# Performance work log

Measured on AMD Instinct MI355X. Metric: run time of the kernel, lower is better.

The kernel has to match this reference:

```python
import jax, jax.numpy as jnp
import numpy as np

# model config (see init_kwargs)
L, H, NH, KVH, DH, I, P, F, T = 8, 1024, 16, 2, 64, 4096, 4, 64, 10
QLEN = 9                      # 1 dit token + P cond tokens + P latent tokens
GROUPS = NH // KVH            # GQA repeat factor
PREFIX = P + 1                # prefix_plus
SCALE = DH ** -0.25           # folded into rope cos/sin (applied to q AND k)


def setup_inputs() -> dict:
    key = jax.random.key(0)
    ks = jax.random.split(key, 16)
    g = lambda i, shape, s=0.02: jax.random.normal(ks[i], shape, jnp.float32) * s
    # sway-sampled timestep schedule -> dt table (matches torch precompute)
    ts = np.linspace(1.0, 0.0, T + 1, dtype=np.float32)
    ts = (ts + 1.0 * (np.cos(np.pi / 2 * ts) - 1.0 + ts))[1:]
    dt_all = jnp.asarray((ts[:-1] - ts[1:]).reshape(1, 1, T - 1))
    # rope tables with attention scale folded in
    pos = np.arange(QLEN, dtype=np.float32)
    inv_freq = 1.0 / (10000.0 ** (np.arange(0, DH, 2, dtype=np.float32) / DH))
    freqs = np.concatenate([np.outer(pos, inv_freq)] * 2, axis=-1)  # [QLEN, DH]
    cos_q = jnp.asarray(np.cos(freqs)[None, None] * SCALE)  # [1,1,QLEN,DH]
    sin_q = jnp.asarray(np.sin(freqs)[None, None] * SCALE)
    return dict(
        random=g(0, (1, P, F), 1.0),
        dit_hidden=g(1, (1, 1, H), 1.0),
        feat_cond=g(2, (2, P, H), 1.0),
        cfg_value=jnp.full((1,), 2.5, jnp.float32),
        cfg_value_minus=jnp.full((1,), -1.5, jnp.float32),
        t_all=g(3, (1, T - 1, H), 1.0),   # precomputed time_mlp output table
        dt_all=dt_all, cos_q=cos_q, sin_q=sin_q,
        W_in=g(4, (F, H)), b_in=jnp.zeros((H,), jnp.float32),
        ln1_w=jnp.ones((L, H), jnp.float32),
        Wq=g(5, (L, H, NH * DH)), Wk=g(6, (L, H, KVH * DH)),
        Wv=g(7, (L, H, KVH * DH)), Wo=g(8, (L, NH * DH, H)),
        ln2_w=jnp.ones((L, H), jnp.float32),
        Wg=g(9, (L, H, I)), Wu=g(10, (L, H, I)), Wd=g(11, (L, I, H)),
        norm_w=jnp.ones((H,), jnp.float32),
        W_out=g(12, (H, F)), b_out=jnp.zeros((F,), jnp.float32),
        step=jnp.zeros((1,), jnp.int32),
    )


def _rms(x, w, eps=1e-6):
    return x * jax.lax.rsqrt(jnp.mean(x * x, axis=-1, keepdims=True) + eps) * w


def _rot_half(x):
    x1, x2 = jnp.split(x, 2, axis=-1)
    return jnp.concatenate([-x2, x1], axis=-1)


def reference(random, dit_hidden, feat_cond, cfg_value, cfg_value_minus,
              t_all, dt_all, cos_q, sin_q, W_in, b_in, ln1_w, Wq, Wk, Wv, Wo,
              ln2_w, Wg, Wu, Wd, norm_w, W_out, b_out, step):
    t = t_all[:, step]                                   # [1,1,H]
    dt = dt_all[..., step]                               # [1,1,1]
    dh = jnp.concatenate([dit_hidden + t, t], axis=0)    # CFG doubling -> [2,1,H]
    x = random @ W_in + b_in                             # [1,P,H]
    h = jnp.concatenate([dh, feat_cond, jnp.concatenate([x, x], axis=0)], axis=1)  # [2,QLEN,H]

    def layer(h, p):
        ln1, wq, wk, wv, wo, ln2, wg, wu, wd = p
        hn = _rms(h, ln1)
        q = (hn @ wq).reshape(2, QLEN, NH, DH).transpose(0, 2, 1, 3)
        k = (hn @ wk).reshape(2, QLEN, KVH, DH).transpose(0, 2, 1, 3)
        v = (hn @ wv).reshape(2, QLEN, KVH, DH).transpose(0, 2, 1, 3)
        # rope with head_dim**-0.25 scale folded into cos/sin (applied to q and k)
        q = q * cos_q + _rot_half(q) * sin_q
        k = k * cos_q + _rot_half(k) * sin_q
        k = jnp.repeat(k, GROUPS, axis=1)                # repeat_k (GQA)
        v = jnp.repeat(v, GROUPS, axis=1)                # repeat_v
        attn = jax.nn.softmax(jnp.einsum('bhqd,bhkd->bhqk', q, k), axis=-1)
        out = jnp.einsum('bhqk,bhkd->bhqd', attn, v)
        out = out.transpose(0, 2, 1, 3).reshape(2, QLEN, NH * DH)
        h = h + out @ wo
        hn2 = _rms(h, ln2)
        h = h + (jax.nn.silu(hn2 @ wg) * (hn2 @ wu)) @ wd
        return h, None

    h, _ = jax.lax.scan(layer, h, (ln1_w, Wq, Wk, Wv, Wo, ln2_w, Wg, Wu, Wd))
    h = _rms(h[:, PREFIX:], norm_w)                      # drop prefix -> [2,P,H]
    out = h @ W_out + b_out                              # [2,P,F]
    pos, neg = out[0:1], out[1:2]
    pf = pos.reshape(1, 1, -1)                           # [1,1,P*F]
    nf = neg.reshape(1, -1, 1)                           # [1,P*F,1]
    st = (pf @ nf) / (jnp.swapaxes(nf, 1, 2) @ nf + 1e-7)  # rescaled CFG, [1,1,1]
    dphi = cfg_value_minus * neg * st + cfg_value * pos
    next_random = random - dt * dphi
    return step + 1, next_random
```

## Files before the change

### kernel.cpp

```cpp
#include <hip/hip_runtime.h>

#define TOKENS 18
#define QLEN 9
#define HDIM 1024
#define IDIM 4096
#define NLAYER 8

#define HA_OFF    0u
#define HB_OFF    18432u
#define SQA_OFF   36864u
#define SQB_OFF   36936u
#define QKVR_OFF  37008u
#define QKVP_OFF  60048u
#define OPP_OFF   797328u
#define GUP_OFF   1387152u
#define M_OFF     3746448u
#define WDP_OFF   3820176u
#define OUTP_OFF  4999824u
#define TOTAL_F   5016208u

__device__ __forceinline__ void loadf2(float2* buf, const float* wp, int base, int stride) {
#pragma unroll
  for (int j = 0; j < 8; j++)
    buf[j] = *reinterpret_cast<const float2*>(wp + (size_t)(base + j) * stride);
}
__device__ __forceinline__ void fmaf2(float2* acc, const float2* buf,
                                      const float (*sb)[TOKENS], int base) {
#pragma unroll
  for (int j = 0; j < 8; j++) {
#pragma unroll
    for (int t = 0; t < TOKENS; t++) {
      float bv = sb[base + j][t];
      acc[t].x += bv * buf[j].x; acc[t].y += bv * buf[j].y;
    }
  }
}
__device__ __forceinline__ void loadf1(float* buf, const float* wp, int base, int stride) {
#pragma unroll
  for (int j = 0; j < 8; j++) buf[j] = wp[(size_t)(base + j) * stride];
}
__device__ __forceinline__ void fmaf1(float* acc, const float* buf,
                                      const float (*sb)[TOKENS], int base) {
#pragma unroll
  for (int j = 0; j < 8; j++) {
#pragma unroll
    for (int t = 0; t < TOKENS; t++) acc[t] += sb[base + j][t] * buf[j];
  }
}

__global__ __launch_bounds__(256) void k_embed(
    const float* __restrict__ rnd, const float* __restrict__ dit,
    const float* __restrict__ feat, const float* __restrict__ t_all,
    const float* __restrict__ W_in, const float* __restrict__ b_in,
    const int* __restrict__ step, float* __restrict__ ws) {
  int t = blockIdx.x >> 2, q4 = blockIdx.x & 3, c0 = q4 * 256;
  int b = t / QLEN, q = t - b * QLEN;
  int tid = threadIdx.x, c = c0 + tid;
  int st = step[0];
  __shared__ float rl[64];
  __shared__ float pr[4];
  float v;
  if (q == 0) {
    v = t_all[(size_t)st * HDIM + c] + (b == 0 ? dit[c] : 0.f);
  } else if (q <= 4) {
    v = feat[(size_t)(b * 4 + q - 1) * HDIM + c];
  } else {
    int p = q - 5;
    if (tid < 64) rl[tid] = rnd[p * 64 + tid];
    __syncthreads();
    float a = b_in[c];
#pragma unroll 8
    for (int f = 0; f < 64; f++) a += rl[f] * W_in[(size_t)f * HDIM + c];
    v = a;
  }
  ws[HA_OFF + (size_t)t * HDIM + c] = v;
  float sq = v * v;
#pragma unroll
  for (int off = 32; off >= 1; off >>= 1) sq += __shfl_down(sq, off);
  if ((tid & 63) == 0) pr[tid >> 6] = sq;
  __syncthreads();
  if (tid == 0) ws[SQA_OFF + (size_t)t * 4 + q4] = pr[0] + pr[1] + pr[2] + pr[3];
}

__global__ __launch_bounds__(256) void k_qkv(
    const float* __restrict__ Wq, const float* __restrict__ Wk,
    const float* __restrict__ Wv, const float* __restrict__ ln1,
    float* __restrict__ ws, int layer) {
  int ks = blockIdx.y, r0 = ks * 32, bx = blockIdx.x, tid = threadIdx.x;
  __shared__ float s_b[32][TOKENS];
  __shared__ float s_rstd[TOKENS];
  if (tid < TOKENS) {
    float s = ws[SQA_OFF + tid * 4] + ws[SQA_OFF + tid * 4 + 1]
            + ws[SQA_OFF + tid * 4 + 2] + ws[SQA_OFF + tid * 4 + 3];
    s_rstd[tid] = rsqrtf(s * (1.f / HDIM) + 1e-6f);
  }
  const float* lw = ln1 + (size_t)layer * HDIM;
  for (int i = tid; i < 576; i += 256) {
    int t = i >> 5, r = i & 31;
    s_b[r][t] = ws[HA_OFF + (size_t)t * HDIM + r0 + r] * lw[r0 + r];
  }
  __syncthreads();
  float* qp = ws + QKVP_OFF + (size_t)ks * (TOKENS * 1280);
  if (bx < 2) {
    int col = bx * 512 + tid * 2;
    const float* wp = Wq + ((size_t)layer << 20) + (size_t)r0 * HDIM + col;
    float2 A[8], B[8];
    float2 acc[TOKENS];
#pragma unroll
    for (int t = 0; t < TOKENS; t++) acc[t] = make_float2(0.f, 0.f);
    loadf2(A, wp, 0, HDIM); loadf2(B, wp, 8, HDIM);
    fmaf2(acc, A, s_b, 0);  loadf2(A, wp, 16, HDIM);
    fmaf2(acc, B, s_b, 8);  loadf2(B, wp, 24, HDIM);
    fmaf2(acc, A, s_b, 16); fmaf2(acc, B, s_b, 24);
#pragma unroll
    for (int t = 0; t < TOKENS; t++) {
      float rs = s_rstd[t];
      *reinterpret_cast<float2*>(qp + (size_t)t * 1280 + col) = make_float2(acc[t].x * rs, acc[t].y * rs);
    }
  } else {
    int c = tid;
    const float* wp = (c < 128)
      ? (Wk + (size_t)layer * 131072 + (size_t)r0 * 128 + c)
      : (Wv + (size_t)layer * 131072 + (size_t)r0 * 128 + (c - 128));
    float A[8], B[8];
    float acc[TOKENS];
#pragma unroll
    for (int t = 0; t < TOKENS; t++) acc[t] = 0.f;
    loadf1(A, wp, 0, 128); loadf1(B, wp, 8, 128);
    fmaf1(acc, A, s_b, 0);  loadf1(A, wp, 16, 128);
    fmaf1(acc, B, s_b, 8);  loadf1(B, wp, 24, 128);
    fmaf1(acc, A, s_b, 16); fmaf1(acc, B, s_b, 24);
#pragma unroll
    for (int t = 0; t < TOKENS; t++) qp[(size_t)t * 1280 + 1024 + c] = acc[t] * s_rstd[t];
  }
}

__global__ __launch_bounds__(256) void k_redq(float* __restrict__ ws) {
  int el = blockIdx.x * 256 + threadIdx.x;
  float s = 0.f;
#pragma unroll 8
  for (int p = 0; p < 32; p++) s += ws[QKVP_OFF + (size_t)p * (TOKENS * 1280) + el];
  ws[QKVR_OFF + el] = s;
}

__global__ __launch_bounds__(256) void k_wo(
    const float* __restrict__ Wo, const float* __restrict__ cosq,
    const float* __restrict__ sinq, float* __restrict__ ws, int layer) {
  const float* qkv = ws + QKVR_OFF;
  int bx = blockIdx.x, by = blockIdx.y, tid = threadIdx.x;
  int r0 = by * 32, head = r0 >> 6, kvh = head >> 3, d0 = r0 & 63;
  __shared__ float lq[2][QLEN][68];
  __shared__ float lk[2][QLEN][68];
  __shared__ float lv[2][QLEN][33];
  __shared__ float sP[2][QLEN][12];
  __shared__ float sA[32][TOKENS];
  for (int i = tid; i < 2 * QLEN * 64; i += 256) {
    int d = i & 63, qi = (i >> 6) % QLEN, b = i / (QLEN * 64);
    const float* qr = qkv + (size_t)(b * QLEN + qi) * 1280;
    float c = cosq[qi * 64 + d], s = sinq[qi * 64 + d];
    float qv = qr[head * 64 + d];
    float qo = (d < 32) ? -qr[head * 64 + d + 32] : qr[head * 64 + d - 32];
    lq[b][qi][d] = qv * c + qo * s;
    float kv = qr[1024 + kvh * 64 + d];
    float ko = (d < 32) ? -qr[1024 + kvh * 64 + d + 32] : qr[1024 + kvh * 64 + d - 32];
    lk[b][qi][d] = kv * c + ko * s;
  }
  for (int i = tid; i < 2 * QLEN * 32; i += 256) {
    int d = i & 31, ki = (i >> 5) % QLEN, b = i / (QLEN * 32);
    lv[b][ki][d] = qkv[(size_t)(b * QLEN + ki) * 1280 + 1152 + kvh * 64 + d0 + d];
  }
  __syncthreads();
  for (int i = tid; i < 2 * QLEN * QLEN; i += 256) {
    int ki = i % QLEN, qi = (i / QLEN) % QLEN, b = i / (QLEN * QLEN);
    float s = 0.f;
#pragma unroll
    for (int d = 0; d < 64; d++) s += lq[b][qi][d] * lk[b][ki][d];
    sP[b][qi][ki] = s;
  }
  __syncthreads();
  if (tid < TOKENS) {
    int b = tid / QLEN, qi = tid % QLEN;
    float m = -1e30f;
#pragma unroll
    for (int k = 0; k < QLEN; k++) m = fmaxf(m, sP[b][qi][k]);
    float e[QLEN], sum = 0.f;
#pragma unroll
    for (int k = 0; k < QLEN; k++) { e[k] = expf(sP[b][qi][k] - m); sum += e[k]; }
    float inv = 1.f / sum;
#pragma unroll
    for (int k = 0; k < QLEN; k++) sP[b][qi][k] = e[k] * inv;
  }
  __syncthreads();
  for (int i = tid; i < 32 * TOKENS; i += 256) {
    int dd = i / TOKENS, t = i - dd * TOKENS;
    int b = t / QLEN, qi = t % QLEN;
    float a = 0.f;
#pragma unroll
    for (int k = 0; k < QLEN; k++) a += sP[b][qi][k] * lv[b][k][dd];
    sA[dd][t] = a;
  }
  __syncthreads();
  int col = bx * 512 + tid * 2;
  const float* wp = Wo + ((size_t)layer << 20) + (size_t)r0 * HDIM + col;
  float2 A[8], B[8];
  float2 acc[TOKENS];
#pragma unroll
  for (int t = 0; t < TOKENS; t++) acc[t] = make_float2(0.f, 0.f);
  loadf2(A, wp, 0, HDIM); loadf2(B, wp, 8, HDIM);
  fmaf2(acc, A, sA, 0);   loadf2(A, wp, 16, HDIM);
  fmaf2(acc, B, sA, 8);   loadf2(B, wp, 24, HDIM);
  fmaf2(acc, A, sA, 16);  fmaf2(acc, B, sA, 24);
  float* op = ws + OPP_OFF + (size_t)by * (TOKENS * HDIM);
#pragma unroll
  for (int t = 0; t < TOKENS; t++)
    *reinterpret_cast<float2*>(op + (size_t)t * HDIM + col) = acc[t];
}

__global__ __launch_bounds__(256) void k_redo(float* __restrict__ ws) {
  int t = blockIdx.x >> 2, q4 = blockIdx.x & 3;
  int tid = threadIdx.x, c = q4 * 256 + tid;
  __shared__ float pr[4];
  float v = ws[HA_OFF + (size_t)t * HDIM + c];
  const float* pp = ws + OPP_OFF + (size_t)t * HDIM + c;
#pragma unroll 8
  for (int p = 0; p < 32; p++) v += pp[(size_t)p * (TOKENS * HDIM)];
  ws[HB_OFF + (size_t)t * HDIM + c] = v;
  float sq = v * v;
#pragma unroll
  for (int off = 32; off >= 1; off >>= 1) sq += __shfl_down(sq, off);
  if ((tid & 63) == 0) pr[tid >> 6] = sq;
  __syncthreads();
  if (tid == 0) ws[SQB_OFF + (size_t)t * 4 + q4] = pr[0] + pr[1] + pr[2] + pr[3];
}

__global__ __launch_bounds__(256) void k_gu(
    const float* __restrict__ Wg, const float* __restrict__ Wu,
    const float* __restrict__ ln2, float* __restrict__ ws, int layer) {
  int cs = blockIdx.x, ks = blockIdx.y, r0 = ks * 64, tid = threadIdx.x;
  __shared__ float s_b[TOKENS][64];
  __shared__ float s_rstd[TOKENS];
  if (tid < TOKENS) {
    float s = ws[SQB_OFF + tid * 4] + ws[SQB_OFF + tid * 4 + 1]
            + ws[SQB_OFF + tid * 4 + 2] + ws[SQB_OFF + tid * 4 + 3];
    s_rstd[tid] = rsqrtf(s * (1.f / HDIM) + 1e-6f);
  }
  const float* lw = ln2 + (size_t)layer * HDIM;
  for (int i = tid; i < TOKENS * 64; i += 256) {
    int t = i >> 6, r = i & 63;
    s_b[t][r] = ws[HB_OFF + (size_t)t * HDIM + r0 + r] * lw[r0 + r];
  }
  __syncthreads();
  const float* W = (cs < 16 ? Wg : Wu) + ((size_t)layer << 22);
  int base = (cs & 15) * 256;
  const float* wp = W + (size_t)r0 * IDIM + base + tid;
  float wbuf[64];
#pragma unroll
  for (int j = 0; j < 64; j++) wbuf[j] = wp[(size_t)j * IDIM];
  float acc[TOKENS];
#pragma unroll
  for (int t = 0; t < TOKENS; t++) acc[t] = 0.f;
#pragma unroll
  for (int j = 0; j < 64; j++) {
#pragma unroll
    for (int t = 0; t < TOKENS; t++) acc[t] += s_b[t][j] * wbuf[j];
  }
  int outcol = (cs < 16 ? base : 4096 + base) + tid;
  float* gp = ws + GUP_OFF + (size_t)ks * (TOKENS * 8192) + outcol;
#pragma unroll
  for (int t = 0; t < TOKENS; t++) gp[(size_t)t * 8192] = acc[t] * s_rstd[t];
}

__global__ __launch_bounds__(256) void k_m(float* __restrict__ ws) {
  int el = blockIdx.x * 256 + threadIdx.x;
  int t = el >> 12, j = el & 4095;
  const float* gp = ws + GUP_OFF + (size_t)t * 8192 + j;
  float g = 0.f, u = 0.f;
#pragma unroll 8
  for (int p = 0; p < 16; p++) {
    g += gp[(size_t)p * (TOKENS * 8192)];
    u += gp[(size_t)p * (TOKENS * 8192) + 4096];
  }
  ws[M_OFF + (size_t)t * 4096 + j] = (g / (1.f + expf(-g))) * u;
}

__global__ __launch_bounds__(256) void k_wd(
    const float* __restrict__ Wd, float* __restrict__ ws, int layer) {
  int ks2 = blockIdx.x >> 3, cs = blockIdx.x & 7;
  int r0 = ks2 * 128, c0 = cs * 128;
  int tid = threadIdx.x, colt = tid & 127, hf = tid >> 7;
  __shared__ float s_b[TOKENS][128];
  for (int i = tid; i < TOKENS * 128; i += 256) {
    int t = i >> 7, r = i & 127;
    s_b[t][r] = ws[M_OFF + (size_t)t * 4096 + r0 + r];
  }
  __syncthreads();
  int col = c0 + colt;
  const float* wp = Wd + ((size_t)layer << 22) + (size_t)(r0 + hf * 64) * HDIM + col;
  float wbuf[64];
#pragma unroll
  for (int j = 0; j < 64; j++) wbuf[j] = wp[(size_t)j * HDIM];
  float acc[TOKENS];
#pragma unroll
  for (int t = 0; t < TOKENS; t++) acc[t] = 0.f;
#pragma unroll
  for (int j = 0; j < 64; j++) {
#pragma unroll
    for (int t = 0; t < TOKENS; t++) acc[t] += s_b[t][hf * 64 + j] * wbuf[j];
  }
  int slab = ks2 * 2 + hf;
  float* wdp = ws + WDP_OFF + (size_t)slab * (TOKENS * HDIM) + col;
#pragma unroll
  for (int t = 0; t < TOKENS; t++) wdp[(size_t)t * HDIM] = acc[t];
}

__global__ __launch_bounds__(256) void k_hup(float* __restrict__ ws) {
  int t = blockIdx.x >> 2, q4 = blockIdx.x & 3;
  int tid = threadIdx.x, c = q4 * 256 + tid;
  __shared__ float pr[4];
  float v = ws[HB_OFF + (size_t)t * HDIM + c];
  const float* pp = ws + WDP_OFF + (size_t)t * HDIM + c;
#pragma unroll 8
  for (int p = 0; p < 64; p++) v += pp[(size_t)p * (TOKENS * HDIM)];
  ws[HA_OFF + (size_t)t * HDIM + c] = v;
  float sq = v * v;
#pragma unroll
  for (int off = 32; off >= 1; off >>= 1) sq += __shfl_down(sq, off);
  if ((tid & 63) == 0) pr[tid >> 6] = sq;
  __syncthreads();
  if (tid == 0) ws[SQA_OFF + (size_t)t * 4 + q4] = pr[0] + pr[1] + pr[2] + pr[3];
}

__global__ __launch_bounds__(256) void k_out(
    const float* __restrict__ Wout, const float* __restrict__ normw,
    float* __restrict__ ws) {
  const float* h = ws + HA_OFF;
  float* outp = ws + OUTP_OFF;
  __shared__ float s_rstd[8];
  __shared__ float s_b[128][8];
  int tid = threadIdx.x;
  if (tid < 8) {
    int tix = (tid >> 2) * QLEN + 5 + (tid & 3);
    float s = ws[SQA_OFF + tix * 4] + ws[SQA_OFF + tix * 4 + 1]
            + ws[SQA_OFF + tix * 4 + 2] + ws[SQA_OFF + tix * 4 + 3];
    s_rstd[tid] = rsqrtf(s * (1.f / HDIM) + 1e-6f);
  }
  __syncthreads();
  int r0 = blockIdx.x * 128;
  for (int i = tid; i < 128 * 8; i += 256) {
    int r = i >> 3, s = i & 7;
    int tix = (s >> 2) * QLEN + 5 + (s & 3);
    s_b[r][s] = h[(size_t)tix * HDIM + r0 + r] * normw[r0 + r] * s_rstd[s];
  }
  __syncthreads();
  int colc = tid & 63, rsub = tid >> 6;
  const float* wp = Wout + (size_t)(r0 + rsub * 32) * 64 + colc;
  float acc[8];
#pragma unroll
  for (int s = 0; s < 8; s++) acc[s] = 0.f;
#pragma unroll 8
  for (int r = 0; r < 32; r++) {
    float w = wp[(size_t)r * 64];
#pragma unroll
    for (int s = 0; s < 8; s++) acc[s] += s_b[rsub * 32 + r][s] * w;
  }
  float* slot = outp + (size_t)(blockIdx.x * 4 + rsub) * 512;
#pragma unroll
  for (int s = 0; s < 8; s++) slot[s * 64 + colc] = acc[s];
}

__global__ __launch_bounds__(256) void k_final(
    const float* __restrict__ rnd, const float* __restrict__ cfg,
    const float* __restrict__ cfgm, const float* __restrict__ dt_all,
    const float* __restrict__ bout, const int* __restrict__ step,
    const float* __restrict__ ws, float* __restrict__ out) {
  const float* outp = ws + OUTP_OFF;
  int tid = threadIdx.x;
  int f = tid & 63;
  float p = bout[f], n = bout[f];
#pragma unroll 8
  for (int pp = 0; pp < 32; pp++) {
    p += outp[(size_t)pp * 512 + tid];
    n += outp[(size_t)pp * 512 + 256 + tid];
  }
  float pn = p * n, nn = n * n;
#pragma unroll
  for (int off = 32; off >= 1; off >>= 1) {
    pn += __shfl_down(pn, off);
    nn += __shfl_down(nn, off);
  }
  __shared__ float red[8];
  __shared__ float s_st;
  int wave = tid >> 6, lane = tid & 63;
  if (lane == 0) { red[wave] = pn; red[4 + wave] = nn; }
  __syncthreads();
  if (tid == 0) {
    float PN = red[0] + red[1] + red[2] + red[3];
    float NN = red[4] + red[5] + red[6] + red[7];
    s_st = PN / (NN + 1e-7f);
  }
  __syncthreads();
  int st = step[0];
  float dphi = cfgm[0] * n * s_st + cfg[0] * p;
  float next = rnd[tid] - dt_all[st] * dphi;
  if (tid == 0) out[0] = (float)(st + 1);
  out[1 + tid] = next;
}

extern "C" void kernel_launch(void* const* d_in, const int* in_sizes, int n_in,
                              void* d_out, int out_size, void* d_ws, size_t ws_size,
                              hipStream_t stream) {
  const float* rnd   = (const float*)d_in[0];
  const float* dit   = (const float*)d_in[1];
  const float* feat  = (const float*)d_in[2];
  const float* cfg   = (const float*)d_in[3];
  const float* cfgm  = (const float*)d_in[4];
  const float* t_all = (const float*)d_in[5];
  const float* dt_al = (const float*)d_in[6];
  const float* cosq  = (const float*)d_in[7];
  const float* sinq  = (const float*)d_in[8];
  const float* W_in  = (const float*)d_in[9];
  const float* b_in  = (const float*)d_in[10];
  const float* ln1   = (const float*)d_in[11];
  const float* Wq    = (const float*)d_in[12];
  const float* Wk    = (const float*)d_in[13];
  const float* Wv    = (const float*)d_in[14];
  const float* Wo    = (const float*)d_in[15];
  const float* ln2   = (const float*)d_in[16];
  const float* Wg    = (const float*)d_in[17];
  const float* Wu    = (const float*)d_in[18];
  const float* Wd    = (const float*)d_in[19];
  const float* normw = (const float*)d_in[20];
  const float* Wout  = (const float*)d_in[21];
  const float* bout  = (const float*)d_in[22];
  const int*   step  = (const int*)d_in[23];
  float* ws = (float*)d_ws;

  k_embed<<<72, 256, 0, stream>>>(rnd, dit, feat, t_all, W_in, b_in, step, ws);
  for (int l = 0; l < NLAYER; l++) {
    k_qkv<<<dim3(3, 32), 256, 0, stream>>>(Wq, Wk, Wv, ln1, ws, l);
    k_redq<<<90, 256, 0, stream>>>(ws);
    k_wo<<<dim3(2, 32), 256, 0, stream>>>(Wo, cosq, sinq, ws, l);
    k_redo<<<72, 256, 0, stream>>>(ws);
    k_gu<<<dim3(32, 16), 256, 0, stream>>>(Wg, Wu, ln2, ws, l);
    k_m<<<288, 256, 0, stream>>>(ws);
    k_wd<<<256, 256, 0, stream>>>(Wd, ws, l);
    k_hup<<<72, 256, 0, stream>>>(ws);
  }
  k_out<<<8, 256, 0, stream>>>(Wout, normw, ws);
  k_final<<<1, 256, 0, stream>>>(rnd, cfg, cfgm, dt_al, bout, step, ws, (float*)d_out);
}
```

Before: 550.3 us.

## Fuse split-K reductions into consumer kernels with in-kernel atomic flag sync

Removes the separate reduction kernels (redq, redo, and per-layer hup). Their work moves into the first 72 blocks of the next kernel, which publish completion through agent-scope atomic counters. The other blocks prefetch their weights into registers before spinning on the counter, so weight loads overlap the reduction. QKV and Wo now use larger 64-row K-slices, giving fewer partials and the wo kernel sums the QKV partials itself. This cuts launches, but it relies on all producer blocks being co-resident or scheduled first to avoid deadlock, and the wider register buffers raise register pressure.

```diff
diff --git a/kernel.cpp b/kernel.cpp
--- a/kernel.cpp
+++ b/kernel.cpp
@@ -10,42 +10,22 @@
 #define HB_OFF    18432u
 #define SQA_OFF   36864u
 #define SQB_OFF   36936u
-#define QKVR_OFF  37008u
-#define QKVP_OFF  60048u
-#define OPP_OFF   797328u
-#define GUP_OFF   1387152u
-#define M_OFF     3746448u
-#define WDP_OFF   3820176u
-#define OUTP_OFF  4999824u
-#define TOTAL_F   5016208u
-
-__device__ __forceinline__ void loadf2(float2* buf, const float* wp, int base, int stride) {
-#pragma unroll
-  for (int j = 0; j < 8; j++)
-    buf[j] = *reinterpret_cast<const float2*>(wp + (size_t)(base + j) * stride);
-}
-__device__ __forceinline__ void fmaf2(float2* acc, const float2* buf,
-                                      const float (*sb)[TOKENS], int base) {
-#pragma unroll
-  for (int j = 0; j < 8; j++) {
-#pragma unroll
-    for (int t = 0; t < TOKENS; t++) {
-      float bv = sb[base + j][t];
-      acc[t].x += bv * buf[j].x; acc[t].y += bv * buf[j].y;
-    }
-  }
-}
-__device__ __forceinline__ void loadf1(float* buf, const float* wp, int base, int stride) {
-#pragma unroll
-  for (int j = 0; j < 8; j++) buf[j] = wp[(size_t)(base + j) * stride];
-}
-__device__ __forceinline__ void fmaf1(float* acc, const float* buf,
-                                      const float (*sb)[TOKENS], int base) {
-#pragma unroll
-  for (int j = 0; j < 8; j++) {
-#pragma unroll
-    for (int t = 0; t < TOKENS; t++) acc[t] += sb[base + j][t] * buf[j];
-  }
+#define CNT_OFF   37008u
+#define QKVP_OFF  37072u
+#define OPP_OFF   405712u
+#define GUP_OFF   700624u
+#define M_OFF     3059920u
+#define WDP_OFF   3133648u
+#define OUTP_OFF  4313296u
+#define TOTAL_F   4329680u
+
+__device__ __forceinline__ void flag_release(unsigned* c) {
+  __threadfence();
+  __hip_atomic_fetch_add(c, 1u, __ATOMIC_RELEASE, __HIP_MEMORY_SCOPE_AGENT);
+}
+__device__ __forceinline__ void flag_spin(unsigned* c, unsigned tgt) {
+  while (__hip_atomic_load(c, __ATOMIC_ACQUIRE, __HIP_MEMORY_SCOPE_AGENT) < tgt)
+    __builtin_amdgcn_s_sleep(2);
 }
 
 __global__ __launch_bounds__(256) void k_embed(
@@ -79,95 +59,122 @@
   for (int off = 32; off >= 1; off >>= 1) sq += __shfl_down(sq, off);
   if ((tid & 63) == 0) pr[tid >> 6] = sq;
   __syncthreads();
-  if (tid == 0) ws[SQA_OFF + (size_t)t * 4 + q4] = pr[0] + pr[1] + pr[2] + pr[3];
+  if (tid == 0) {
+    ws[SQA_OFF + (size_t)t * 4 + q4] = pr[0] + pr[1] + pr[2] + pr[3];
+    flag_release((unsigned*)(ws + CNT_OFF) + 0);
+  }
 }
 
 __global__ __launch_bounds__(256) void k_qkv(
     const float* __restrict__ Wq, const float* __restrict__ Wk,
     const float* __restrict__ Wv, const float* __restrict__ ln1,
     float* __restrict__ ws, int layer) {
-  int ks = blockIdx.y, r0 = ks * 32, bx = blockIdx.x, tid = threadIdx.x;
-  __shared__ float s_b[32][TOKENS];
+  int bx = blockIdx.x, ks = blockIdx.y, r0 = ks * 64, tid = threadIdx.x;
+  int id = ks * 5 + bx;
+  unsigned* cnt = (unsigned*)(ws + CNT_OFF) + layer;
+  __shared__ float s_b[64][TOKENS];
   __shared__ float s_rstd[TOKENS];
+  __shared__ float pr[4];
+  if (layer > 0 && id < 72) {
+    int t = id >> 2, q4 = id & 3, c = q4 * 256 + tid;
+    float v = ws[HB_OFF + (size_t)t * HDIM + c];
+    const float* pp = ws + WDP_OFF + (size_t)t * HDIM + c;
+#pragma unroll 8
+    for (int p = 0; p < 64; p++) v += pp[(size_t)p * (TOKENS * HDIM)];
+    ws[HA_OFF + (size_t)t * HDIM + c] = v;
+    float sq = v * v;
+#pragma unroll
+    for (int off = 32; off >= 1; off >>= 1) sq += __shfl_down(sq, off);
+    if ((tid & 63) == 0) pr[tid >> 6] = sq;
+    __syncthreads();
+    if (tid == 0) {
+      ws[SQA_OFF + (size_t)t * 4 + q4] = pr[0] + pr[1] + pr[2] + pr[3];
+      flag_release(cnt);
+    }
+  }
+  float W[64];
+  const float* wp;
+  int stride;
+  int col = 0;
+  if (bx < 4) {
+    col = bx * 256 + tid;
+    wp = Wq + ((size_t)layer << 20) + (size_t)r0 * HDIM + col;
+    stride = HDIM;
+  } else {
+    wp = (tid < 128)
+       ? (Wk + (size_t)layer * 131072 + (size_t)r0 * 128 + tid)
+       : (Wv + (size_t)layer * 131072 + (size_t)r0 * 128 + (tid - 128));
+    stride = 128;
+  }
+#pragma unroll
+  for (int j = 0; j < 64; j++) W[j] = wp[(size_t)j * stride];
+  if (tid == 0) flag_spin(cnt, 72u);
+  __syncthreads();
   if (tid < TOKENS) {
     float s = ws[SQA_OFF + tid * 4] + ws[SQA_OFF + tid * 4 + 1]
             + ws[SQA_OFF + tid * 4 + 2] + ws[SQA_OFF + tid * 4 + 3];
     s_rstd[tid] = rsqrtf(s * (1.f / HDIM) + 1e-6f);
   }
   const float* lw = ln1 + (size_t)layer * HDIM;
-  for (int i = tid; i < 576; i += 256) {
-    int t = i >> 5, r = i & 31;
+  for (int i = tid; i < 64 * TOKENS; i += 256) {
+    int t = i % TOKENS, r = i / TOKENS;
     s_b[r][t] = ws[HA_OFF + (size_t)t * HDIM + r0 + r] * lw[r0 + r];
   }
   __syncthreads();
+  float acc[TOKENS];
+#pragma unroll
+  for (int t = 0; t < TOKENS; t++) acc[t] = 0.f;
+#pragma unroll
+  for (int j = 0; j < 64; j++) {
+#pragma unroll
+    for (int t = 0; t < TOKENS; t++) acc[t] += s_b[j][t] * W[j];
+  }
   float* qp = ws + QKVP_OFF + (size_t)ks * (TOKENS * 1280);
-  if (bx < 2) {
-    int col = bx * 512 + tid * 2;
-    const float* wp = Wq + ((size_t)layer << 20) + (size_t)r0 * HDIM + col;
-    float2 A[8], B[8];
-    float2 acc[TOKENS];
-#pragma unroll
-    for (int t = 0; t < TOKENS; t++) acc[t] = make_float2(0.f, 0.f);
-    loadf2(A, wp, 0, HDIM); loadf2(B, wp, 8, HDIM);
-    fmaf2(acc, A, s_b, 0);  loadf2(A, wp, 16, HDIM);
-    fmaf2(acc, B, s_b, 8);  loadf2(B, wp, 24, HDIM);
-    fmaf2(acc, A, s_b, 16); fmaf2(acc, B, s_b, 24);
-#pragma unroll
-    for (int t = 0; t < TOKENS; t++) {
-      float rs = s_rstd[t];
-      *reinterpret_cast<float2*>(qp + (size_t)t * 1280 + col) = make_float2(acc[t].x * rs, acc[t].y * rs);
-    }
+  if (bx < 4) {
+#pragma unroll
+    for (int t = 0; t < TOKENS; t++) qp[(size_t)t * 1280 + col] = acc[t] * s_rstd[t];
   } else {
-    int c = tid;
-    const float* wp = (c < 128)
-      ? (Wk + (size_t)layer * 131072 + (size_t)r0 * 128 + c)
-      : (Wv + (size_t)layer * 131072 + (size_t)r0 * 128 + (c - 128));
-    float A[8], B[8];
-    float acc[TOKENS];
-#pragma unroll
-    for (int t = 0; t < TOKENS; t++) acc[t] = 0.f;
-    loadf1(A, wp, 0, 128); loadf1(B, wp, 8, 128);
-    fmaf1(acc, A, s_b, 0);  loadf1(A, wp, 16, 128);
-    fmaf1(acc, B, s_b, 8);  loadf1(B, wp, 24, 128);
-    fmaf1(acc, A, s_b, 16); fmaf1(acc, B, s_b, 24);
-#pragma unroll
-    for (int t = 0; t < TOKENS; t++) qp[(size_t)t * 1280 + 1024 + c] = acc[t] * s_rstd[t];
-  }
-}
-
-__global__ __launch_bounds__(256) void k_redq(float* __restrict__ ws) {
-  int el = blockIdx.x * 256 + threadIdx.x;
-  float s = 0.f;
-#pragma unroll 8
-  for (int p = 0; p < 32; p++) s += ws[QKVP_OFF + (size_t)p * (TOKENS * 1280) + el];
-  ws[QKVR_OFF + el] = s;
+#pragma unroll
+    for (int t = 0; t < TOKENS; t++) qp[(size_t)t * 1280 + 1024 + tid] = acc[t] * s_rstd[t];
+  }
 }
 
 __global__ __launch_bounds__(256) void k_wo(
     const float* __restrict__ Wo, const float* __restrict__ cosq,
     const float* __restrict__ sinq, float* __restrict__ ws, int layer) {
-  const float* qkv = ws + QKVR_OFF;
   int bx = blockIdx.x, by = blockIdx.y, tid = threadIdx.x;
-  int r0 = by * 32, head = r0 >> 6, kvh = head >> 3, d0 = r0 & 63;
+  int head = by, kvh = head >> 3;
   __shared__ float lq[2][QLEN][68];
   __shared__ float lk[2][QLEN][68];
-  __shared__ float lv[2][QLEN][33];
+  __shared__ float lv[2][QLEN][68];
   __shared__ float sP[2][QLEN][12];
-  __shared__ float sA[32][TOKENS];
+  __shared__ float sA[64][TOKENS];
   for (int i = tid; i < 2 * QLEN * 64; i += 256) {
     int d = i & 63, qi = (i >> 6) % QLEN, b = i / (QLEN * 64);
-    const float* qr = qkv + (size_t)(b * QLEN + qi) * 1280;
-    float c = cosq[qi * 64 + d], s = sinq[qi * 64 + d];
-    float qv = qr[head * 64 + d];
-    float qo = (d < 32) ? -qr[head * 64 + d + 32] : qr[head * 64 + d - 32];
-    lq[b][qi][d] = qv * c + qo * s;
-    float kv = qr[1024 + kvh * 64 + d];
-    float ko = (d < 32) ? -qr[1024 + kvh * 64 + d + 32] : qr[1024 + kvh * 64 + d - 32];
-    lk[b][qi][d] = kv * c + ko * s;
-  }
+    const float* base = ws + QKVP_OFF + (size_t)(b * QLEN + qi) * 1280;
+    float qs = 0.f, ks2 = 0.f, vs = 0.f;
+#pragma unroll 8
+    for (int p = 0; p < 16; p++) {
+      const float* sp = base + (size_t)p * (TOKENS * 1280);
+      qs  += sp[head * 64 + d];
+      ks2 += sp[1024 + kvh * 64 + d];
+      vs  += sp[1152 + kvh * 64 + d];
+    }
+    lq[b][qi][d] = qs;
+    lk[b][qi][d] = ks2;
+    lv[b][qi][d] = vs;
+  }
+  __syncthreads();
   for (int i = tid; i < 2 * QLEN * 32; i += 256) {
-    int d = i & 31, ki = (i >> 5) % QLEN, b = i / (QLEN * 32);
-    lv[b][ki][d] = qkv[(size_t)(b * QLEN + ki) * 1280 + 1152 + kvh * 64 + d0 + d];
+    int d = i & 31, qi = (i >> 5) % QLEN, b = i / (QLEN * 32);
+    float c1 = cosq[qi * 64 + d],      s1 = sinq[qi * 64 + d];
+    float c2 = cosq[qi * 64 + 32 + d], s2 = sinq[qi * 64 + 32 + d];
+    float qa = lq[b][qi][d], qb = lq[b][qi][32 + d];
+    lq[b][qi][d]      = qa * c1 - qb * s1;
+    lq[b][qi][32 + d] = qb * c2 + qa * s2;
+    float ka = lk[b][qi][d], kb = lk[b][qi][32 + d];
+    lk[b][qi][d]      = ka * c1 - kb * s1;
+    lk[b][qi][32 + d] = kb * c2 + ka * s2;
   }
   __syncthreads();
   for (int i = tid; i < 2 * QLEN * QLEN; i += 256) {
@@ -191,8 +198,8 @@
     for (int k = 0; k < QLEN; k++) sP[b][qi][k] = e[k] * inv;
   }
   __syncthreads();
-  for (int i = tid; i < 32 * TOKENS; i += 256) {
-    int dd = i / TOKENS, t = i - dd * TOKENS;
+  for (int i = tid; i < 64 * TOKENS; i += 256) {
+    int dd = i / TOKENS, t = i % TOKENS;
     int b = t / QLEN, qi = t % QLEN;
     float a = 0.f;
 #pragma unroll
@@ -200,45 +207,58 @@
     sA[dd][t] = a;
   }
   __syncthreads();
-  int col = bx * 512 + tid * 2;
-  const float* wp = Wo + ((size_t)layer << 20) + (size_t)r0 * HDIM + col;
-  float2 A[8], B[8];
-  float2 acc[TOKENS];
-#pragma unroll
-  for (int t = 0; t < TOKENS; t++) acc[t] = make_float2(0.f, 0.f);
-  loadf2(A, wp, 0, HDIM); loadf2(B, wp, 8, HDIM);
-  fmaf2(acc, A, sA, 0);   loadf2(A, wp, 16, HDIM);
-  fmaf2(acc, B, sA, 8);   loadf2(B, wp, 24, HDIM);
-  fmaf2(acc, A, sA, 16);  fmaf2(acc, B, sA, 24);
+  int col = bx * 256 + tid;
+  const float* wp = Wo + ((size_t)layer << 20) + (size_t)(head * 64) * HDIM + col;
+  float W[64];
+#pragma unroll
+  for (int j = 0; j < 64; j++) W[j] = wp[(size_t)j * HDIM];
+  float acc[TOKENS];
+#pragma unroll
+  for (int t = 0; t < TOKENS; t++) acc[t] = 0.f;
+#pragma unroll
+  for (int j = 0; j < 64; j++) {
+#pragma unroll
+    for (int t = 0; t < TOKENS; t++) acc[t] += sA[j][t] * W[j];
+  }
   float* op = ws + OPP_OFF + (size_t)by * (TOKENS * HDIM);
 #pragma unroll
-  for (int t = 0; t < TOKENS; t++)
-    *reinterpret_cast<float2*>(op + (size_t)t * HDIM + col) = acc[t];
-}
-
-__global__ __launch_bounds__(256) void k_redo(float* __restrict__ ws) {
-  int t = blockIdx.x >> 2, q4 = blockIdx.x & 3;
-  int tid = threadIdx.x, c = q4 * 256 + tid;
-  __shared__ float pr[4];
-  float v = ws[HA_OFF + (size_t)t * HDIM + c];
-  const float* pp = ws + OPP_OFF + (size_t)t * HDIM + c;
-#pragma unroll 8
-  for (int p = 0; p < 32; p++) v += pp[(size_t)p * (TOKENS * HDIM)];
-  ws[HB_OFF + (size_t)t * HDIM + c] = v;
-  float sq = v * v;
-#pragma unroll
-  for (int off = 32; off >= 1; off >>= 1) sq += __shfl_down(sq, off);
-  if ((tid & 63) == 0) pr[tid >> 6] = sq;
-  __syncthreads();
-  if (tid == 0) ws[SQB_OFF + (size_t)t * 4 + q4] = pr[0] + pr[1] + pr[2] + pr[3];
-}
-
-__global__ __launch_bounds__(256) void k_gu(
+  for (int t = 0; t < TOKENS; t++) op[(size_t)t * HDIM + col] = acc[t];
+}
+
+__global__ __launch_bounds__(256, 2) void k_gu(
     const float* __restrict__ Wg, const float* __restrict__ Wu,
     const float* __restrict__ ln2, float* __restrict__ ws, int layer) {
-  int cs = blockIdx.x, ks = blockIdx.y, r0 = ks * 64, tid = threadIdx.x;
+  int bid = blockIdx.x, tid = threadIdx.x;
+  int cs = bid >> 4, ks = bid & 15, r0 = ks * 64;
+  unsigned* cnt = (unsigned*)(ws + CNT_OFF) + 8 + layer;
   __shared__ float s_b[TOKENS][64];
   __shared__ float s_rstd[TOKENS];
+  __shared__ float pr[4];
+  if (bid < 72) {
+    int t = bid >> 2, q4 = bid & 3, c = q4 * 256 + tid;
+    float v = ws[HA_OFF + (size_t)t * HDIM + c];
+    const float* pp = ws + OPP_OFF + (size_t)t * HDIM + c;
+#pragma unroll 8
+    for (int p = 0; p < 16; p++) v += pp[(size_t)p * (TOKENS * HDIM)];
+    ws[HB_OFF + (size_t)t * HDIM + c] = v;
+    float sq = v * v;
+#pragma unroll
+    for (int off = 32; off >= 1; off >>= 1) sq += __shfl_down(sq, off);
+    if ((tid & 63) == 0) pr[tid >> 6] = sq;
+    __syncthreads();
+    if (tid == 0) {
+      ws[SQB_OFF + (size_t)t * 4 + q4] = pr[0] + pr[1] + pr[2] + pr[3];
+      flag_release(cnt);
+    }
+  }
+  int base = (cs & 15) * 256;
+  const float* W = (cs < 16 ? Wg : Wu) + ((size_t)layer << 22);
+  const float* wp = W + (size_t)r0 * IDIM + base + tid;
+  float wbuf[64];
+#pragma unroll
+  for (int j = 0; j < 64; j++) wbuf[j] = wp[(size_t)j * IDIM];
+  if (tid == 0) flag_spin(cnt, 72u);
+  __syncthreads();
   if (tid < TOKENS) {
     float s = ws[SQB_OFF + tid * 4] + ws[SQB_OFF + tid * 4 + 1]
             + ws[SQB_OFF + tid * 4 + 2] + ws[SQB_OFF + tid * 4 + 3];
@@ -250,12 +270,6 @@
     s_b[t][r] = ws[HB_OFF + (size_t)t * HDIM + r0 + r] * lw[r0 + r];
   }
   __syncthreads();
-  const float* W = (cs < 16 ? Wg : Wu) + ((size_t)layer << 22);
-  int base = (cs & 15) * 256;
-  const float* wp = W + (size_t)r0 * IDIM + base + tid;
-  float wbuf[64];
-#pragma unroll
-  for (int j = 0; j < 64; j++) wbuf[j] = wp[(size_t)j * IDIM];
   float acc[TOKENS];
 #pragma unroll
   for (int t = 0; t < TOKENS; t++) acc[t] = 0.f;
@@ -435,17 +449,17 @@
   const int*   step  = (const int*)d_in[23];
   float* ws = (float*)d_ws;
 
+  hipMemsetAsync((void*)(ws + CNT_OFF), 0, 64 * sizeof(unsigned), stream);
+
   k_embed<<<72, 256, 0, stream>>>(rnd, dit, feat, t_all, W_in, b_in, step, ws);
   for (int l = 0; l < NLAYER; l++) {
-    k_qkv<<<dim3(3, 32), 256, 0, stream>>>(Wq, Wk, Wv, ln1, ws, l);
-    k_redq<<<90, 256, 0, stream>>>(ws);
-    k_wo<<<dim3(2, 32), 256, 0, stream>>>(Wo, cosq, sinq, ws, l);
-    k_redo<<<72, 256, 0, stream>>>(ws);
-    k_gu<<<dim3(32, 16), 256, 0, stream>>>(Wg, Wu, ln2, ws, l);
+    k_qkv<<<dim3(5, 16), 256, 0, stream>>>(Wq, Wk, Wv, ln1, ws, l);
+    k_wo<<<dim3(4, 16), 256, 0, stream>>>(Wo, cosq, sinq, ws, l);
+    k_gu<<<512, 256, 0, stream>>>(Wg, Wu, ln2, ws, l);
     k_m<<<288, 256, 0, stream>>>(ws);
     k_wd<<<256, 256, 0, stream>>>(Wd, ws, l);
-    k_hup<<<72, 256, 0, stream>>>(ws);
-  }
+  }
+  k_hup<<<72, 256, 0, stream>>>(ws);
   k_out<<<8, 256, 0, stream>>>(Wout, normw, ws);
   k_final<<<1, 256, 0, stream>>>(rnd, cfg, cfgm, dt_al, bout, step, ws, (float*)d_out);
 }
```

After: 821.3 us. 1.49x slower.

## Fold split-K reductions into GEMV kernels and fuse SiLU-gate into down-proj

Applied to the files above, without the earlier changes.

The QKV, gate/up and down projection kernels now have each block stage the full normalized activation vector in LDS and reduce over K inside the block, using wave shuffles and a small LDS reduction. This removes the separate split-K partial-sum kernels (k_redq, k_m) and shrinks the partial buffers. The SiLU*up product is now computed inside k_wd from the gate/up outputs. The cost is that every block reloads and renormalizes the whole 1024x18 activation tile into about 72KB of LDS, which limits occupancy and duplicates that prologue work. Weight reads also move to 16-column-wide strided patterns with less coalescing per row.

```diff
diff --git a/kernel.cpp b/kernel.cpp
--- a/kernel.cpp
+++ b/kernel.cpp
@@ -11,13 +11,11 @@
 #define SQA_OFF   36864u
 #define SQB_OFF   36936u
 #define QKVR_OFF  37008u
-#define QKVP_OFF  60048u
-#define OPP_OFF   797328u
-#define GUP_OFF   1387152u
-#define M_OFF     3746448u
-#define WDP_OFF   3820176u
-#define OUTP_OFF  4999824u
-#define TOTAL_F   5016208u
+#define OPP_OFF   60048u
+#define GU_OFF    649872u
+#define WDP_OFF   797328u
+#define OUTP_OFF  871056u
+#define TOTAL_F   887440u
 
 __device__ __forceinline__ void loadf2(float2* buf, const float* wp, int base, int stride) {
 #pragma unroll
@@ -33,18 +31,6 @@
       float bv = sb[base + j][t];
       acc[t].x += bv * buf[j].x; acc[t].y += bv * buf[j].y;
     }
-  }
-}
-__device__ __forceinline__ void loadf1(float* buf, const float* wp, int base, int stride) {
-#pragma unroll
-  for (int j = 0; j < 8; j++) buf[j] = wp[(size_t)(base + j) * stride];
-}
-__device__ __forceinline__ void fmaf1(float* acc, const float* buf,
-                                      const float (*sb)[TOKENS], int base) {
-#pragma unroll
-  for (int j = 0; j < 8; j++) {
-#pragma unroll
-    for (int t = 0; t < TOKENS; t++) acc[t] += sb[base + j][t] * buf[j];
   }
 }
 
@@ -86,61 +72,62 @@
     const float* __restrict__ Wq, const float* __restrict__ Wk,
     const float* __restrict__ Wv, const float* __restrict__ ln1,
     float* __restrict__ ws, int layer) {
-  int ks = blockIdx.y, r0 = ks * 32, bx = blockIdx.x, tid = threadIdx.x;
-  __shared__ float s_b[32][TOKENS];
+  int blk = blockIdx.x, tid = threadIdx.x;
+  int seg = tid >> 4, col = tid & 15;
+  __shared__ float hn[1024 * TOKENS];
+  __shared__ float red[4 * 16 * TOKENS];
   __shared__ float s_rstd[TOKENS];
   if (tid < TOKENS) {
     float s = ws[SQA_OFF + tid * 4] + ws[SQA_OFF + tid * 4 + 1]
             + ws[SQA_OFF + tid * 4 + 2] + ws[SQA_OFF + tid * 4 + 3];
     s_rstd[tid] = rsqrtf(s * (1.f / HDIM) + 1e-6f);
   }
+  __syncthreads();
   const float* lw = ln1 + (size_t)layer * HDIM;
-  for (int i = tid; i < 576; i += 256) {
-    int t = i >> 5, r = i & 31;
-    s_b[r][t] = ws[HA_OFF + (size_t)t * HDIM + r0 + r] * lw[r0 + r];
-  }
-  __syncthreads();
-  float* qp = ws + QKVP_OFF + (size_t)ks * (TOKENS * 1280);
-  if (bx < 2) {
-    int col = bx * 512 + tid * 2;
-    const float* wp = Wq + ((size_t)layer << 20) + (size_t)r0 * HDIM + col;
-    float2 A[8], B[8];
-    float2 acc[TOKENS];
-#pragma unroll
-    for (int t = 0; t < TOKENS; t++) acc[t] = make_float2(0.f, 0.f);
-    loadf2(A, wp, 0, HDIM); loadf2(B, wp, 8, HDIM);
-    fmaf2(acc, A, s_b, 0);  loadf2(A, wp, 16, HDIM);
-    fmaf2(acc, B, s_b, 8);  loadf2(B, wp, 24, HDIM);
-    fmaf2(acc, A, s_b, 16); fmaf2(acc, B, s_b, 24);
-#pragma unroll
-    for (int t = 0; t < TOKENS; t++) {
-      float rs = s_rstd[t];
-      *reinterpret_cast<float2*>(qp + (size_t)t * 1280 + col) = make_float2(acc[t].x * rs, acc[t].y * rs);
+#pragma unroll 2
+  for (int t = 0; t < TOKENS; t++) {
+    float rs = s_rstd[t];
+    for (int row = tid; row < 1024; row += 256)
+      hn[row * TOKENS + t] = ws[HA_OFF + (size_t)t * HDIM + row] * lw[row] * rs;
+  }
+  __syncthreads();
+  int c0 = blk * 16;
+  const float* wp; int stride;
+  if (c0 < 1024)      { wp = Wq + ((size_t)layer << 20) + (size_t)(seg * 64) * 1024 + c0 + col; stride = 1024; }
+  else if (c0 < 1152) { wp = Wk + (size_t)layer * 131072 + (size_t)(seg * 64) * 128 + (c0 - 1024) + col; stride = 128; }
+  else                { wp = Wv + (size_t)layer * 131072 + (size_t)(seg * 64) * 128 + (c0 - 1152) + col; stride = 128; }
+  float acc[TOKENS];
+#pragma unroll
+  for (int t = 0; t < TOKENS; t++) acc[t] = 0.f;
+#pragma unroll
+  for (int jc = 0; jc < 8; jc++) {
+    float wb[8];
+#pragma unroll
+    for (int j = 0; j < 8; j++) wb[j] = wp[(size_t)(jc * 8 + j) * stride];
+#pragma unroll
+    for (int j = 0; j < 8; j++) {
+      const float* hr = &hn[(seg * 64 + jc * 8 + j) * TOKENS];
+#pragma unroll
+      for (int t = 0; t < TOKENS; t++) acc[t] += hr[t] * wb[j];
     }
-  } else {
-    int c = tid;
-    const float* wp = (c < 128)
-      ? (Wk + (size_t)layer * 131072 + (size_t)r0 * 128 + c)
-      : (Wv + (size_t)layer * 131072 + (size_t)r0 * 128 + (c - 128));
-    float A[8], B[8];
-    float acc[TOKENS];
-#pragma unroll
-    for (int t = 0; t < TOKENS; t++) acc[t] = 0.f;
-    loadf1(A, wp, 0, 128); loadf1(B, wp, 8, 128);
-    fmaf1(acc, A, s_b, 0);  loadf1(A, wp, 16, 128);
-    fmaf1(acc, B, s_b, 8);  loadf1(B, wp, 24, 128);
-    fmaf1(acc, A, s_b, 16); fmaf1(acc, B, s_b, 24);
-#pragma unroll
-    for (int t = 0; t < TOKENS; t++) qp[(size_t)t * 1280 + 1024 + c] = acc[t] * s_rstd[t];
-  }
-}
-
-__global__ __launch_bounds__(256) void k_redq(float* __restrict__ ws) {
-  int el = blockIdx.x * 256 + threadIdx.x;
-  float s = 0.f;
-#pragma unroll 8
-  for (int p = 0; p < 32; p++) s += ws[QKVP_OFF + (size_t)p * (TOKENS * 1280) + el];
-  ws[QKVR_OFF + el] = s;
+  }
+#pragma unroll
+  for (int t = 0; t < TOKENS; t++) {
+    acc[t] += __shfl_down(acc[t], 32);
+    acc[t] += __shfl_down(acc[t], 16);
+  }
+  int lane = tid & 63, wv = tid >> 6;
+  if (lane < 16) {
+#pragma unroll
+    for (int t = 0; t < TOKENS; t++) red[(wv * 16 + lane) * TOKENS + t] = acc[t];
+  }
+  __syncthreads();
+  for (int i = tid; i < 16 * TOKENS; i += 256) {
+    int c = i & 15, t = i >> 4;
+    float s = red[(0 * 16 + c) * TOKENS + t] + red[(1 * 16 + c) * TOKENS + t]
+            + red[(2 * 16 + c) * TOKENS + t] + red[(3 * 16 + c) * TOKENS + t];
+    ws[QKVR_OFF + (size_t)t * 1280 + c0 + c] = s;
+  }
 }
 
 __global__ __launch_bounds__(256) void k_wo(
@@ -233,84 +220,116 @@
   if (tid == 0) ws[SQB_OFF + (size_t)t * 4 + q4] = pr[0] + pr[1] + pr[2] + pr[3];
 }
 
-__global__ __launch_bounds__(256) void k_gu(
+__global__ __launch_bounds__(256) void k_gum(
     const float* __restrict__ Wg, const float* __restrict__ Wu,
     const float* __restrict__ ln2, float* __restrict__ ws, int layer) {
-  int cs = blockIdx.x, ks = blockIdx.y, r0 = ks * 64, tid = threadIdx.x;
-  __shared__ float s_b[TOKENS][64];
+  int b = blockIdx.x, tid = threadIdx.x;
+  int mat = b >> 8, j0 = (b & 255) * 16;
+  int seg = tid >> 4, col = tid & 15;
+  __shared__ float hn[1024 * TOKENS];
+  __shared__ float red[4 * 16 * TOKENS];
   __shared__ float s_rstd[TOKENS];
   if (tid < TOKENS) {
     float s = ws[SQB_OFF + tid * 4] + ws[SQB_OFF + tid * 4 + 1]
             + ws[SQB_OFF + tid * 4 + 2] + ws[SQB_OFF + tid * 4 + 3];
     s_rstd[tid] = rsqrtf(s * (1.f / HDIM) + 1e-6f);
   }
+  __syncthreads();
   const float* lw = ln2 + (size_t)layer * HDIM;
-  for (int i = tid; i < TOKENS * 64; i += 256) {
-    int t = i >> 6, r = i & 63;
-    s_b[t][r] = ws[HB_OFF + (size_t)t * HDIM + r0 + r] * lw[r0 + r];
-  }
-  __syncthreads();
-  const float* W = (cs < 16 ? Wg : Wu) + ((size_t)layer << 22);
-  int base = (cs & 15) * 256;
-  const float* wp = W + (size_t)r0 * IDIM + base + tid;
-  float wbuf[64];
-#pragma unroll
-  for (int j = 0; j < 64; j++) wbuf[j] = wp[(size_t)j * IDIM];
+#pragma unroll 2
+  for (int t = 0; t < TOKENS; t++) {
+    float rs = s_rstd[t];
+    for (int row = tid; row < 1024; row += 256)
+      hn[row * TOKENS + t] = ws[HB_OFF + (size_t)t * HDIM + row] * lw[row] * rs;
+  }
+  __syncthreads();
+  const float* wp = (mat ? Wu : Wg) + ((size_t)layer << 22)
+                  + (size_t)(seg * 64) * IDIM + j0 + col;
   float acc[TOKENS];
 #pragma unroll
   for (int t = 0; t < TOKENS; t++) acc[t] = 0.f;
 #pragma unroll
-  for (int j = 0; j < 64; j++) {
-#pragma unroll
-    for (int t = 0; t < TOKENS; t++) acc[t] += s_b[t][j] * wbuf[j];
-  }
-  int outcol = (cs < 16 ? base : 4096 + base) + tid;
-  float* gp = ws + GUP_OFF + (size_t)ks * (TOKENS * 8192) + outcol;
-#pragma unroll
-  for (int t = 0; t < TOKENS; t++) gp[(size_t)t * 8192] = acc[t] * s_rstd[t];
-}
-
-__global__ __launch_bounds__(256) void k_m(float* __restrict__ ws) {
-  int el = blockIdx.x * 256 + threadIdx.x;
-  int t = el >> 12, j = el & 4095;
-  const float* gp = ws + GUP_OFF + (size_t)t * 8192 + j;
-  float g = 0.f, u = 0.f;
-#pragma unroll 8
-  for (int p = 0; p < 16; p++) {
-    g += gp[(size_t)p * (TOKENS * 8192)];
-    u += gp[(size_t)p * (TOKENS * 8192) + 4096];
-  }
-  ws[M_OFF + (size_t)t * 4096 + j] = (g / (1.f + expf(-g))) * u;
+  for (int jc = 0; jc < 8; jc++) {
+    float wb[8];
+#pragma unroll
+    for (int j = 0; j < 8; j++) wb[j] = wp[(size_t)(jc * 8 + j) * IDIM];
+#pragma unroll
+    for (int j = 0; j < 8; j++) {
+      const float* hr = &hn[(seg * 64 + jc * 8 + j) * TOKENS];
+#pragma unroll
+      for (int t = 0; t < TOKENS; t++) acc[t] += hr[t] * wb[j];
+    }
+  }
+#pragma unroll
+  for (int t = 0; t < TOKENS; t++) {
+    acc[t] += __shfl_down(acc[t], 32);
+    acc[t] += __shfl_down(acc[t], 16);
+  }
+  int lane = tid & 63, wv = tid >> 6;
+  if (lane < 16) {
+#pragma unroll
+    for (int t = 0; t < TOKENS; t++) red[(wv * 16 + lane) * TOKENS + t] = acc[t];
+  }
+  __syncthreads();
+  for (int i = tid; i < 16 * TOKENS; i += 256) {
+    int c = i & 15, t = i >> 4;
+    float s = red[(0 * 16 + c) * TOKENS + t] + red[(1 * 16 + c) * TOKENS + t]
+            + red[(2 * 16 + c) * TOKENS + t] + red[(3 * 16 + c) * TOKENS + t];
+    ws[GU_OFF + (size_t)t * 8192 + mat * 4096 + j0 + c] = s;
+  }
 }
 
 __global__ __launch_bounds__(256) void k_wd(
     const float* __restrict__ Wd, float* __restrict__ ws, int layer) {
-  int ks2 = blockIdx.x >> 3, cs = blockIdx.x & 7;
-  int r0 = ks2 * 128, c0 = cs * 128;
-  int tid = threadIdx.x, colt = tid & 127, hf = tid >> 7;
-  __shared__ float s_b[TOKENS][128];
-  for (int i = tid; i < TOKENS * 128; i += 256) {
-    int t = i >> 7, r = i & 127;
-    s_b[t][r] = ws[M_OFF + (size_t)t * 4096 + r0 + r];
-  }
-  __syncthreads();
-  int col = c0 + colt;
-  const float* wp = Wd + ((size_t)layer << 22) + (size_t)(r0 + hf * 64) * HDIM + col;
-  float wbuf[64];
-#pragma unroll
-  for (int j = 0; j < 64; j++) wbuf[j] = wp[(size_t)j * HDIM];
+  int b = blockIdx.x, tid = threadIdx.x;
+  int kc = b >> 6, cc = b & 63;
+  int k0 = kc * 1024, c0 = cc * 16;
+  int seg = tid >> 4, col = tid & 15;
+  __shared__ float mt[1024 * TOKENS];
+  __shared__ float red[4 * 16 * TOKENS];
+#pragma unroll 2
+  for (int t = 0; t < TOKENS; t++) {
+    for (int row = tid; row < 1024; row += 256) {
+      float g = ws[GU_OFF + (size_t)t * 8192 + k0 + row];
+      float u = ws[GU_OFF + (size_t)t * 8192 + 4096 + k0 + row];
+      mt[row * TOKENS + t] = (g / (1.f + expf(-g))) * u;
+    }
+  }
+  __syncthreads();
+  const float* wp = Wd + ((size_t)layer << 22)
+                  + (size_t)(k0 + seg * 64) * HDIM + c0 + col;
   float acc[TOKENS];
 #pragma unroll
   for (int t = 0; t < TOKENS; t++) acc[t] = 0.f;
 #pragma unroll
-  for (int j = 0; j < 64; j++) {
-#pragma unroll
-    for (int t = 0; t < TOKENS; t++) acc[t] += s_b[t][hf * 64 + j] * wbuf[j];
-  }
-  int slab = ks2 * 2 + hf;
-  float* wdp = ws + WDP_OFF + (size_t)slab * (TOKENS * HDIM) + col;
-#pragma unroll
-  for (int t = 0; t < TOKENS; t++) wdp[(size_t)t * HDIM] = acc[t];
+  for (int jc = 0; jc < 8; jc++) {
+    float wb[8];
+#pragma unroll
+    for (int j = 0; j < 8; j++) wb[j] = wp[(size_t)(jc * 8 + j) * HDIM];
+#pragma unroll
+    for (int j = 0; j < 8; j++) {
+      const float* hr = &mt[(seg * 64 + jc * 8 + j) * TOKENS];
+#pragma unroll
+      for (int t = 0; t < TOKENS; t++) acc[t] += hr[t] * wb[j];
+    }
+  }
+#pragma unroll
+  for (int t = 0; t < TOKENS; t++) {
+    acc[t] += __shfl_down(acc[t], 32);
+    acc[t] += __shfl_down(acc[t], 16);
+  }
+  int lane = tid & 63, wv = tid >> 6;
+  if (lane < 16) {
+#pragma unroll
+    for (int t = 0; t < TOKENS; t++) red[(wv * 16 + lane) * TOKENS + t] = acc[t];
+  }
+  __syncthreads();
+  for (int i = tid; i < 16 * TOKENS; i += 256) {
+    int c = i & 15, t = i >> 4;
+    float s = red[(0 * 16 + c) * TOKENS + t] + red[(1 * 16 + c) * TOKENS + t]
+            + red[(2 * 16 + c) * TOKENS + t] + red[(3 * 16 + c) * TOKENS + t];
+    ws[WDP_OFF + (size_t)kc * (TOKENS * HDIM) + (size_t)t * HDIM + c0 + c] = s;
+  }
 }
 
 __global__ __launch_bounds__(256) void k_hup(float* __restrict__ ws) {
@@ -319,8 +338,8 @@
   __shared__ float pr[4];
   float v = ws[HB_OFF + (size_t)t * HDIM + c];
   const float* pp = ws + WDP_OFF + (size_t)t * HDIM + c;
-#pragma unroll 8
-  for (int p = 0; p < 64; p++) v += pp[(size_t)p * (TOKENS * HDIM)];
+#pragma unroll
+  for (int p = 0; p < 4; p++) v += pp[(size_t)p * (TOKENS * HDIM)];
   ws[HA_OFF + (size_t)t * HDIM + c] = v;
   float sq = v * v;
 #pragma unroll
@@ -437,12 +456,10 @@
 
   k_embed<<<72, 256, 0, stream>>>(rnd, dit, feat, t_all, W_in, b_in, step, ws);
   for (int l = 0; l < NLAYER; l++) {
-    k_qkv<<<dim3(3, 32), 256, 0, stream>>>(Wq, Wk, Wv, ln1, ws, l);
-    k_redq<<<90, 256, 0, stream>>>(ws);
+    k_qkv<<<80, 256, 0, stream>>>(Wq, Wk, Wv, ln1, ws, l);
     k_wo<<<dim3(2, 32), 256, 0, stream>>>(Wo, cosq, sinq, ws, l);
     k_redo<<<72, 256, 0, stream>>>(ws);
-    k_gu<<<dim3(32, 16), 256, 0, stream>>>(Wg, Wu, ln2, ws, l);
-    k_m<<<288, 256, 0, stream>>>(ws);
+    k_gum<<<512, 256, 0, stream>>>(Wg, Wu, ln2, ws, l);
     k_wd<<<256, 256, 0, stream>>>(Wd, ws, l);
     k_hup<<<72, 256, 0, stream>>>(ws);
   }
```

Measured after the change: 925.3 us. 68.2% more time.
